# Performance work log

Hardware: AMD Instinct MI355X
Metric: run time of the kernel (lower is better)

Reference implementation:

```python
import jax, jax.numpy as jnp
import numpy as np

N, E, CIN, CHID, DIM, KS = 6000, 192000, 32, 64, 3, 5
K = KS ** DIM          # 125 total spline kernel weights
S = 2 ** DIM           # 8 nonzero linear B-spline basis products per edge


def spline_conv(x, edge_index, pseudo, W, root, bias):
    """SplineConv, degree-1 open B-spline, mean aggregation, root weight + bias.
    x: [N, Cin], edge_index: [2, E], pseudo: [E, DIM] in [0,1],
    W: [K, Cin, Cout], root: [Cin, Cout], bias: [Cout].
    """
    src, dst = edge_index[0], edge_index[1]
    cin = x.shape[1]
    # open spline: KS-1 intervals over [0,1]
    u = pseudo * (KS - 1)                               # [E, DIM]
    i0 = jnp.clip(jnp.floor(u), 0, KS - 2).astype(jnp.int32)
    frac = u - i0                                       # [E, DIM]
    bits = (jnp.arange(S)[:, None] >> jnp.arange(DIM)[None, :]) & 1   # [S, DIM]
    strides = KS ** jnp.arange(DIM - 1, -1, -1)         # row-major flattening
    idx = jnp.sum((i0[:, None, :] + bits[None, :, :]) * strides, axis=-1)  # [E, S]
    basis = jnp.prod(jnp.where(bits[None, :, :] == 1,
                               frac[:, None, :], 1.0 - frac[:, None, :]), axis=-1)  # [E, S]
    x_j = x[src]                                        # gather: [E, Cin]
    vals = (basis[..., None] * x_j[:, None, :]).reshape(E * S, cin)
    keys = (dst[:, None] * K + idx).reshape(E * S)
    # bucket basis-weighted source features per (dst node, kernel index)
    T = jax.ops.segment_sum(vals, keys, num_segments=N * K).reshape(N, K, cin)
    out = jnp.einsum('nki,kio->no', T, W)               # [N, Cout]
    deg = jax.ops.segment_sum(jnp.ones((E,), jnp.float32), dst, num_segments=N)
    out = out / jnp.maximum(deg, 1.0)[:, None]          # mean aggregation
    return out + x @ root + bias


def _conv_params(key, cin):
    k1, k2 = jax.random.split(key)
    w_scale = 1.0 / np.sqrt(cin * S)
    W = jax.random.normal(k1, (K, cin, CHID), jnp.float32) * w_scale
    root = jax.random.normal(k2, (cin, CHID), jnp.float32) * (1.0 / np.sqrt(cin))
    b = jnp.zeros((CHID,), jnp.float32)
    return W, root, b


def setup_inputs() -> dict:
    key = jax.random.key(0)
    ks = jax.random.split(key, 10)
    inp = {
        'x': jax.random.normal(ks[0], (N, CIN), jnp.float32),
        'hidden': jax.random.normal(ks[1], (N, CHID), jnp.float32),
        'edge_index': jax.random.randint(ks[2], (2, E), 0, N, dtype=jnp.int32),
        'edge_attr': jax.random.uniform(ks[3], (E, DIM), jnp.float32),
    }
    for i, (name, cin) in enumerate([('xr', CIN), ('hr', CHID), ('xz', CIN),
                                     ('hz', CHID), ('xn', CIN), ('hn', CHID)]):
        W, root, b = _conv_params(ks[4 + i], cin)
        inp[f'W_{name}'] = W
        inp[f'root_{name}'] = root
        inp[f'b_{name}'] = b
    return inp


def reference(x, hidden, edge_index, edge_attr,
              W_xr, root_xr, b_xr, W_hr, root_hr, b_hr,
              W_xz, root_xz, b_xz, W_hz, root_hz, b_hz,
              W_xn, root_xn, b_xn, W_hn, root_hn, b_hn):
    hr_out = spline_conv(hidden, edge_index, edge_attr, W_hr, root_hr, b_hr)
    r = jax.nn.sigmoid(spline_conv(x, edge_index, edge_attr, W_xr, root_xr, b_xr) + hr_out)
    z = jax.nn.sigmoid(spline_conv(x, edge_index, edge_attr, W_xz, root_xz, b_xz)
                       + spline_conv(hidden, edge_index, edge_attr, W_hz, root_hz, b_hz))
    # NOTE: the original torch forward reuses self.hr (not self.hn) here; replicated faithfully.
    n = jnp.tanh(spline_conv(x, edge_index, edge_attr, W_xn, root_xn, b_xn) + r * hr_out)
    h_new = (1.0 - z) * n + z * hidden
    return h_new
```

## Files before the change

### kernel.cpp

```cpp
#include <hip/hip_runtime.h>
#include <math.h>

#define NN_   6000
#define EE_   192000
#define CIN_  32
#define CHID_ 64
#define KK_   125
#define EB_   32
#define CH1_  4
#define CH2_  8
#define CPB_  16
#define MTILE_ 192

static __device__ __forceinline__ unsigned short f2bf(float f) {
    unsigned int u = __builtin_bit_cast(unsigned int, f);
    u += 0x7fff + ((u >> 16) & 1);
    return (unsigned short)(u >> 16);
}
static __device__ __forceinline__ float bf2f(unsigned short h) {
    unsigned int u = ((unsigned int)h) << 16;
    return __builtin_bit_cast(float, u);
}

#define PK1_ (192 * KK_ * CIN_)
#define PK2_ (128 * KK_ * CHID_)
#define CB_  ((EE_ + 255) / 256)
__global__ __launch_bounds__(256) void count_pack_kernel(
    const int* __restrict__ ei, int* __restrict__ deg,
    const float* __restrict__ W_xr, const float* __restrict__ W_xz,
    const float* __restrict__ W_xn, const float* __restrict__ W_hr,
    const float* __restrict__ W_hz,
    unsigned short* __restrict__ B1t, unsigned short* __restrict__ B2t)
{
    const int b = blockIdx.x;
    if (b < CB_) {
        int e = b * 256 + threadIdx.x;
        if (e < EE_) atomicAdd(&deg[ei[EE_ + e]], 1);
        return;
    }
    int gid = (b - CB_) * 256 + threadIdx.x;
    if (gid < PK1_) {
        int n  = gid / (KK_ * CIN_);
        int kk = gid % (KK_ * CIN_);
        int conv = n >> 6, o = n & 63;
        const float* W = (conv == 0) ? W_xr : ((conv == 1) ? W_xz : W_xn);
        B1t[gid] = f2bf(W[(size_t)kk * 64 + o]);
    } else if (gid < PK1_ + PK2_) {
        int g2 = gid - PK1_;
        int n  = g2 / (KK_ * CHID_);
        int kk = g2 % (KK_ * CHID_);
        int conv = n >> 6, o = n & 63;
        const float* W = (conv == 0) ? W_hr : W_hz;
        B2t[g2] = f2bf(W[(size_t)kk * 64 + o]);
    }
}

__global__ __launch_bounds__(1024) void scan_kernel(
    const int* __restrict__ deg, int* __restrict__ offs, int* __restrict__ cursor)
{
    __shared__ int part[1024];
    const int tid = threadIdx.x;
    const int CH = (NN_ + 1023) / 1024;
    const int base = tid * CH;
    int loc[CH];
    int s = 0;
#pragma unroll
    for (int i = 0; i < CH; ++i) {
        int v = (base + i < NN_) ? deg[base + i] : 0;
        loc[i] = s; s += v;
    }
    part[tid] = s;
    __syncthreads();
    for (int off = 1; off < 1024; off <<= 1) {
        int v = (tid >= off) ? part[tid - off] : 0;
        __syncthreads();
        part[tid] += v;
        __syncthreads();
    }
    const int pre = (tid > 0) ? part[tid - 1] : 0;
#pragma unroll
    for (int i = 0; i < CH; ++i) {
        if (base + i < NN_) {
            offs[base + i]   = pre + loc[i];
            cursor[base + i] = pre + loc[i];
        }
    }
    if (tid == 1023) offs[NN_] = part[1023];
}

__global__ __launch_bounds__(256) void prep_kernel(
    const int* __restrict__ ei, const float* __restrict__ attr,
    int* __restrict__ cursor, float4* __restrict__ meta_s, int* __restrict__ src_s)
{
    int e = blockIdx.x * 256 + threadIdx.x;
    if (e >= EE_) return;
    const int dst = ei[EE_ + e];
    const int p   = atomicAdd(&cursor[dst], 1);
    float f[3]; int i0[3];
#pragma unroll
    for (int d = 0; d < 3; ++d) {
        float u  = attr[e * 3 + d] * 4.0f;
        float fl = floorf(u);
        fl = fminf(fmaxf(fl, 0.0f), 3.0f);
        i0[d] = (int)fl;
        f[d]  = u - fl;
    }
    meta_s[p] = make_float4(f[0], f[1], f[2],
        __int_as_float(i0[0] * 25 + i0[1] * 5 + i0[2]));
    src_s[p] = ei[e];
}

template<int C>
__global__ __launch_bounds__(256) void build_T_kernel(
    const float4* __restrict__ meta_s, const int* __restrict__ src_s,
    const float* __restrict__ feat, const int* __restrict__ offs,
    unsigned short* __restrict__ Tb)
{
    constexpr int MP  = 40;
    constexpr int CT  = C / 16;
    constexpr int CPT = C / 8;
    using bf16x8 = __attribute__((ext_vector_type(8))) short;
    using f32x4  = __attribute__((ext_vector_type(4))) float;

    __shared__ __align__(16) unsigned short Mt [128 * MP];
    __shared__ __align__(16) unsigned short fbT[C   * MP];
    __shared__ int s_src[EB_];

    const int tid  = threadIdx.x;
    const int wave = tid >> 6;
    const int lane = tid & 63;
    const int quad = lane >> 4;
    const int l16  = lane & 15;
    const int node = blockIdx.x;

    for (int i = tid; i < C * MP / 8; i += 256)
        ((uint4*)fbT)[i] = make_uint4(0u, 0u, 0u, 0u);

    const int j0 = offs[node], j1 = offs[node + 1];

    f32x4 acc[2][CT];
#pragma unroll
    for (int t = 0; t < 2; ++t)
#pragma unroll
        for (int ct = 0; ct < CT; ++ct) acc[t][ct] = (f32x4){0.f, 0.f, 0.f, 0.f};

    for (int jb = j0; jb < j1; jb += EB_) {
        const int m = min(EB_, j1 - jb);

        __syncthreads();
        for (int i = tid; i < 128 * MP / 8; i += 256)
            ((uint4*)Mt)[i] = make_uint4(0u, 0u, 0u, 0u);
        if (tid < m) s_src[tid] = src_s[jb + tid];
        __syncthreads();

        if (tid < m) {
            const float4 mt = meta_s[jb + tid];
            const int base = __float_as_int(mt.w);
            const float f0 = mt.x, f1 = mt.y, f2 = mt.z;
            const float g0 = 1.f - f0, g1 = 1.f - f1, g2 = 1.f - f2;
            const float bb[8] = {g0*g1*g2, f0*g1*g2, g0*f1*g2, f0*f1*g2,
                                 g0*g1*f2, f0*g1*f2, g0*f1*f2, f0*f1*f2};
            const int oc[8] = {0, 25, 5, 30, 1, 26, 6, 31};
#pragma unroll
            for (int s = 0; s < 8; ++s)
                Mt[(base + oc[s]) * MP + tid] = f2bf(bb[s]);
        }
        {
            const int e = tid >> 3, cg = (tid & 7) * CPT;
            if (e < m) {
                const float* fr = &feat[(size_t)s_src[e] * C + cg];
#pragma unroll
                for (int c4 = 0; c4 < CPT; c4 += 4) {
                    float4 v = *(const float4*)(fr + c4);
                    fbT[(cg + c4 + 0) * MP + e] = f2bf(v.x);
                    fbT[(cg + c4 + 1) * MP + e] = f2bf(v.y);
                    fbT[(cg + c4 + 2) * MP + e] = f2bf(v.z);
                    fbT[(cg + c4 + 3) * MP + e] = f2bf(v.w);
                }
            }
        }
        __syncthreads();

        bf16x8 a0 = *(const bf16x8*)&Mt[((wave * 2 + 0) * 16 + l16) * MP + quad * 8];
        bf16x8 a1 = *(const bf16x8*)&Mt[((wave * 2 + 1) * 16 + l16) * MP + quad * 8];
#pragma unroll
        for (int ct = 0; ct < CT; ++ct) {
            bf16x8 b = *(const bf16x8*)&fbT[(ct * 16 + l16) * MP + quad * 8];
            acc[0][ct] = __builtin_amdgcn_mfma_f32_16x16x32_bf16(a0, b, acc[0][ct], 0, 0, 0);
            acc[1][ct] = __builtin_amdgcn_mfma_f32_16x16x32_bf16(a1, b, acc[1][ct], 0, 0, 0);
        }
    }

    unsigned short* To = Tb + (size_t)node * (KK_ * C);
#pragma unroll
    for (int t = 0; t < 2; ++t) {
        const int rbase = (wave * 2 + t) * 16 + quad * 4;
#pragma unroll
        for (int ct = 0; ct < CT; ++ct) {
#pragma unroll
            for (int r = 0; r < 4; ++r) {
                const int R = rbase + r;
                if (R < KK_) To[R * C + ct * 16 + l16] = f2bf(acc[t][ct][r]);
            }
        }
    }
}

template<int NT, int NTF, int CPB>
static __device__ __forceinline__ void gemm_body(
    unsigned char* arena,
    const unsigned short* __restrict__ A, const unsigned short* __restrict__ Bt,
    unsigned short* __restrict__ P, int M, int Kd, int chunk, int zhalf)
{
    constexpr int COLS   = 64;
    constexpr int RF     = 3;
    constexpr int NFRAG  = NT / 16;
    constexpr int CSP    = NT + 8;
    constexpr int ABYTES = MTILE_ * COLS * 2;
    constexpr int BBYTES = NT * COLS * 2;
    constexpr int AUNITS = MTILE_ * COLS / 8;
    constexpr int BUNITS = NT * COLS / 8;

    using bf16x8 = __attribute__((ext_vector_type(8))) short;
    using f32x4  = __attribute__((ext_vector_type(4))) float;

    unsigned short* As0 = (unsigned short*)(arena);
    unsigned short* As1 = (unsigned short*)(arena + ABYTES);
    unsigned short* Bs0 = (unsigned short*)(arena + 2 * ABYTES);
    unsigned short* Bs1 = (unsigned short*)(arena + 2 * ABYTES + BBYTES);

    const int tid  = threadIdx.x;
    const int wave = tid >> 6;
    const int lane = tid & 63;
    const int quad = lane >> 4;
    const int l16  = lane & 15;
    const int m0   = blockIdx.x * MTILE_;
    const unsigned short* Bp = Bt + (size_t)zhalf * NT * Kd;
    const int kbase = chunk * CPB * COLS;
    const int ccmax = min(CPB, (Kd - kbase + COLS - 1) / COLS);

    f32x4 acc[RF][NFRAG];
#pragma unroll
    for (int t = 0; t < RF; ++t)
#pragma unroll
        for (int f = 0; f < NFRAG; ++f) acc[t][f] = (f32x4){0.f, 0.f, 0.f, 0.f};

    auto STAGE = [&](int cc, unsigned short* Abuf, unsigned short* Bbuf) {
        const int k0 = kbase + cc * COLS;
#pragma unroll
        for (int i = 0; i < AUNITS / 256; ++i) {
            const int u    = tid + i * 256;
            const int row  = u >> 3;
            const int gblk = (u & 7) ^ (row & 7);
            const int k    = k0 + gblk * 8;
            if (k + 8 <= Kd) {
                const unsigned short* g = A + (size_t)(m0 + row) * Kd + k;
                __builtin_amdgcn_global_load_lds(
                    (const __attribute__((address_space(1))) void*)g,
                    (__attribute__((address_space(3))) void*)(Abuf + u * 8),
                    16, 0, 0);
            } else {
                *(uint4*)(Abuf + u * 8) = make_uint4(0u, 0u, 0u, 0u);
            }
        }
#pragma unroll
        for (int i = 0; i < BUNITS / 256; ++i) {
            const int u    = tid + i * 256;
            const int row  = u >> 3;
            const int gblk = (u & 7) ^ (row & 7);
            const unsigned short* g = Bp + (size_t)row * Kd + k0 + gblk * 8;
            __builtin_amdgcn_global_load_lds(
                (const __attribute__((address_space(1))) void*)g,
                (__attribute__((address_space(3))) void*)(Bbuf + u * 8),
                16, 0, 0);
        }
    };

    STAGE(0, As0, Bs0);
    __syncthreads();

    for (int cc = 0; cc < ccmax; ++cc) {
        unsigned short* Ac = (cc & 1) ? As1 : As0;
        unsigned short* Bc = (cc & 1) ? Bs1 : Bs0;
        if (cc + 1 < ccmax)
            STAGE(cc + 1, (cc & 1) ? As0 : As1, (cc & 1) ? Bs0 : Bs1);
#pragma unroll
        for (int s = 0; s < 2; ++s) {
            bf16x8 av[RF];
#pragma unroll
            for (int t = 0; t < RF; ++t) {
                const int row = (wave * RF + t) * 16 + l16;
                av[t] = *(const bf16x8*)
                    &Ac[row * COLS + (((s * 4 + quad) ^ (l16 & 7)) * 8)];
            }
#pragma unroll
            for (int f = 0; f < NFRAG; ++f) {
                bf16x8 bv = *(const bf16x8*)
                    &Bc[(f * 16 + l16) * COLS + (((s * 4 + quad) ^ (l16 & 7)) * 8)];
#pragma unroll
                for (int t = 0; t < RF; ++t)
                    acc[t][f] = __builtin_amdgcn_mfma_f32_16x16x32_bf16(
                        av[t], bv, acc[t][f], 0, 0, 0);
            }
        }
        __syncthreads();
    }

    unsigned short* Cs = (unsigned short*)arena;
    unsigned short* Pc = P + ((size_t)chunk * M + m0) * NTF + zhalf * NT;
#pragma unroll
    for (int p = 0; p < 3; ++p) {
        __syncthreads();
#pragma unroll
        for (int t = 0; t < RF; ++t) {
            const int fr = wave * RF + t;
            if ((fr >> 2) == p) {
                const int rb = (fr & 3) * 16 + quad * 4;
#pragma unroll
                for (int f = 0; f < NFRAG; ++f) {
                    const int col = f * 16 + l16;
#pragma unroll
                    for (int r = 0; r < 4; ++r)
                        Cs[(rb + r) * CSP + col] = f2bf(acc[t][f][r]);
                }
            }
        }
        __syncthreads();
        constexpr int UNITS = 64 * NT / 8;
        for (int u = tid; u < UNITS; u += 256) {
            const int row = (u * 8) / NT, col = (u * 8) % NT;
            if (m0 + p * 64 + row < M)
                *(uint4*)&Pc[(size_t)(p * 64 + row) * NTF + col] =
                    *(const uint4*)&Cs[row * CSP + col];
        }
    }
}

__global__ __launch_bounds__(256) void gemm_all_kernel(
    const unsigned short* __restrict__ Tx, const unsigned short* __restrict__ B1t,
    unsigned short* __restrict__ P1,
    const unsigned short* __restrict__ Th, const unsigned short* __restrict__ B2t,
    unsigned short* __restrict__ P2)
{
    __shared__ __align__(16) unsigned char arena[2 * 24576 + 2 * 16384];
    const int y = blockIdx.y;
    if (y < CH2_) {
        gemm_body<128, 128, CPB_>(arena, Th, B2t, P2, NN_, KK_ * CHID_, y, 0);
    } else {
        const int g = y - CH2_;
        gemm_body<96, 192, CPB_>(arena, Tx, B1t, P1, NN_, KK_ * CIN_, g >> 1, g & 1);
    }
}

__global__ __launch_bounds__(256) void epilogue_kernel(
    const unsigned short* __restrict__ P1, const unsigned short* __restrict__ P2,
    const int* __restrict__ offs,
    const float* __restrict__ x, const float* __restrict__ hidden,
    const float* __restrict__ root_xr, const float* __restrict__ root_hr,
    const float* __restrict__ root_xz, const float* __restrict__ root_hz,
    const float* __restrict__ root_xn,
    const float* __restrict__ b_xr, const float* __restrict__ b_hr,
    const float* __restrict__ b_xz, const float* __restrict__ b_hz,
    const float* __restrict__ b_xn,
    float* __restrict__ out)
{
    __shared__ float xsh[4][32];
    __shared__ float hsh[4][64];
    const int w = threadIdx.x >> 6;
    const int o = threadIdx.x & 63;
    const int m = blockIdx.x * 4 + w;
    if (m >= NN_) return;

    if (o < 32) xsh[w][o] = x[(size_t)m * 32 + o];
    const float hval = hidden[(size_t)m * 64 + o];
    hsh[w][o] = hval;

    float axr = 0.f, axz = 0.f, axn = 0.f;
#pragma unroll
    for (int c = 0; c < CH1_; ++c) {
        const unsigned short* p = P1 + ((size_t)c * NN_ + m) * 192;
        axr += bf2f(p[o]); axz += bf2f(p[64 + o]); axn += bf2f(p[128 + o]);
    }
    float ahr = 0.f, ahz = 0.f;
#pragma unroll
    for (int c = 0; c < CH2_; ++c) {
        const unsigned short* p = P2 + ((size_t)c * NN_ + m) * 128;
        ahr += bf2f(p[o]); ahz += bf2f(p[64 + o]);
    }

    const int   dg   = offs[m + 1] - offs[m];
    const float dinv = 1.0f / fmaxf((float)dg, 1.0f);
    axr *= dinv; axz *= dinv; axn *= dinv; ahr *= dinv; ahz *= dinv;

    float sxr = 0.f, sxz = 0.f, sxn = 0.f;
#pragma unroll
    for (int c = 0; c < CIN_; ++c) {
        float xv = xsh[w][c];
        sxr += xv * root_xr[c * 64 + o];
        sxz += xv * root_xz[c * 64 + o];
        sxn += xv * root_xn[c * 64 + o];
    }
    float shr = 0.f, shz = 0.f;
#pragma unroll
    for (int c = 0; c < CHID_; ++c) {
        float hv = hsh[w][c];
        shr += hv * root_hr[c * 64 + o];
        shz += hv * root_hz[c * 64 + o];
    }

    const float conv_xr = axr + sxr + b_xr[o];
    const float conv_xz = axz + sxz + b_xz[o];
    const float conv_xn = axn + sxn + b_xn[o];
    const float hr_out  = ahr + shr + b_hr[o];
    const float conv_hz = ahz + shz + b_hz[o];

    const float rg = 1.0f / (1.0f + expf(-(conv_xr + hr_out)));
    const float zg = 1.0f / (1.0f + expf(-(conv_xz + conv_hz)));
    const float ng = tanhf(conv_xn + rg * hr_out);
    out[(size_t)m * 64 + o] = (1.0f - zg) * ng + zg * hval;
}

extern "C" void kernel_launch(void* const* d_in, const int* in_sizes, int n_in,
                              void* d_out, int out_size, void* d_ws, size_t ws_size,
                              hipStream_t stream)
{
    const float* x       = (const float*)d_in[0];
    const float* hidden  = (const float*)d_in[1];
    const int*   ei      = (const int*)  d_in[2];
    const float* attr    = (const float*)d_in[3];
    const float* W_xr    = (const float*)d_in[4];
    const float* root_xr = (const float*)d_in[5];
    const float* b_xr    = (const float*)d_in[6];
    const float* W_hr    = (const float*)d_in[7];
    const float* root_hr = (const float*)d_in[8];
    const float* b_hr    = (const float*)d_in[9];
    const float* W_xz    = (const float*)d_in[10];
    const float* root_xz = (const float*)d_in[11];
    const float* b_xz    = (const float*)d_in[12];
    const float* W_hz    = (const float*)d_in[13];
    const float* root_hz = (const float*)d_in[14];
    const float* b_hz    = (const float*)d_in[15];
    const float* W_xn    = (const float*)d_in[16];
    const float* root_xn = (const float*)d_in[17];
    const float* b_xn    = (const float*)d_in[18];
    float* out = (float*)d_out;

    char* w = (char*)d_ws;
    unsigned short* Tx  = (unsigned short*)w; w += (size_t)NN_ * KK_ * CIN_  * 2;
    unsigned short* Th  = (unsigned short*)w; w += (size_t)NN_ * KK_ * CHID_ * 2;
    unsigned short* B1t = (unsigned short*)w; w += (size_t)192 * KK_ * CIN_  * 2;
    unsigned short* B2t = (unsigned short*)w; w += (size_t)128 * KK_ * CHID_ * 2;
    unsigned short* P1  = (unsigned short*)w; w += (size_t)CH1_ * NN_ * 192 * 2;
    unsigned short* P2  = (unsigned short*)w; w += (size_t)CH2_ * NN_ * 128 * 2;
    float4* meta_s = (float4*)w; w += (size_t)EE_ * 16;
    int* src_s  = (int*)w;   w += (size_t)EE_ * 4;
    int* deg    = (int*)w;   w += (size_t)NN_ * 4;
    int* offs   = (int*)w;   w += (size_t)(NN_ + 4) * 4;
    int* cursor = (int*)w;   w += (size_t)NN_ * 4;

    const int MT = (NN_ + MTILE_ - 1) / MTILE_;

    hipMemsetAsync(deg, 0, (size_t)NN_ * 4, stream);

    const int PACKB = (PK1_ + PK2_ + 255) / 256;
    count_pack_kernel<<<CB_ + PACKB, 256, 0, stream>>>(
        ei, deg, W_xr, W_xz, W_xn, W_hr, W_hz, B1t, B2t);

    scan_kernel<<<1, 1024, 0, stream>>>(deg, offs, cursor);
    prep_kernel<<<(EE_ + 255) / 256, 256, 0, stream>>>(ei, attr, cursor, meta_s, src_s);

    build_T_kernel<CHID_><<<NN_, 256, 0, stream>>>(meta_s, src_s, hidden, offs, Th);
    build_T_kernel<CIN_><<<NN_, 256, 0, stream>>>(meta_s, src_s, x, offs, Tx);

    gemm_all_kernel<<<dim3(MT, CH2_ + 2 * CH1_), 256, 0, stream>>>(
        Tx, B1t, P1, Th, B2t, P2);

    epilogue_kernel<<<(NN_ + 3) / 4, 256, 0, stream>>>(
        P1, P2, offs, x, hidden,
        root_xr, root_hr, root_xz, root_hz, root_xn,
        b_xr, b_hr, b_xz, b_hz, b_xn, out);
}
```

Before: 249.9 us.

## Triple-buffer GEMM LDS staging with explicit vmcnt waits and zero-pad loads

The GEMM main loop moves from double buffering to a three-slot LDS ring with two stages in flight. It uses explicit s_waitcnt vmcnt counts plus raw barriers in place of __syncthreads. Out-of-range A tiles now load from a zeroed global pad through global_load_lds instead of writing zeros to LDS directly, which keeps the per-stage load count uniform for the vmcnt arithmetic. This is meant to hide global-to-LDS latency better, at the cost of more LDS per block (about 120KB), which may lower occupancy, and the fragility of hand-counted wait values.

```diff
diff --git a/kernel.cpp b/kernel.cpp
--- a/kernel.cpp
+++ b/kernel.cpp
@@ -20,6 +20,11 @@
 static __device__ __forceinline__ float bf2f(unsigned short h) {
     unsigned int u = ((unsigned int)h) << 16;
     return __builtin_bit_cast(float, u);
+}
+
+template<int N> static __device__ __forceinline__ void vwait() {
+    asm volatile("s_waitcnt vmcnt(%0)" :: "n"(N) : "memory");
+    __builtin_amdgcn_sched_barrier(0);
 }
 
 #define PK1_ (192 * KK_ * CIN_)
@@ -206,28 +211,24 @@
     }
 }
 
-template<int NT, int NTF, int CPB>
+template<int NT, int NTF, int CPB, int LW>
 static __device__ __forceinline__ void gemm_body(
-    unsigned char* arena,
+    unsigned short* arena,
     const unsigned short* __restrict__ A, const unsigned short* __restrict__ Bt,
+    const unsigned short* __restrict__ zp,
     unsigned short* __restrict__ P, int M, int Kd, int chunk, int zhalf)
 {
     constexpr int COLS   = 64;
     constexpr int RF     = 3;
     constexpr int NFRAG  = NT / 16;
     constexpr int CSP    = NT + 8;
-    constexpr int ABYTES = MTILE_ * COLS * 2;
-    constexpr int BBYTES = NT * COLS * 2;
+    constexpr int ASH    = MTILE_ * COLS;
+    constexpr int SLOT   = ASH + 128 * COLS;
     constexpr int AUNITS = MTILE_ * COLS / 8;
     constexpr int BUNITS = NT * COLS / 8;
 
     using bf16x8 = __attribute__((ext_vector_type(8))) short;
     using f32x4  = __attribute__((ext_vector_type(4))) float;
-
-    unsigned short* As0 = (unsigned short*)(arena);
-    unsigned short* As1 = (unsigned short*)(arena + ABYTES);
-    unsigned short* Bs0 = (unsigned short*)(arena + 2 * ABYTES);
-    unsigned short* Bs1 = (unsigned short*)(arena + 2 * ABYTES + BBYTES);
 
     const int tid  = threadIdx.x;
     const int wave = tid >> 6;
@@ -245,7 +246,9 @@
 #pragma unroll
         for (int f = 0; f < NFRAG; ++f) acc[t][f] = (f32x4){0.f, 0.f, 0.f, 0.f};
 
-    auto STAGE = [&](int cc, unsigned short* Abuf, unsigned short* Bbuf) {
+    auto STAGE = [&](int cc, int slot) {
+        unsigned short* Abuf = arena + slot * SLOT;
+        unsigned short* Bbuf = Abuf + ASH;
         const int k0 = kbase + cc * COLS;
 #pragma unroll
         for (int i = 0; i < AUNITS / 256; ++i) {
@@ -253,15 +256,13 @@
             const int row  = u >> 3;
             const int gblk = (u & 7) ^ (row & 7);
             const int k    = k0 + gblk * 8;
-            if (k + 8 <= Kd) {
-                const unsigned short* g = A + (size_t)(m0 + row) * Kd + k;
-                __builtin_amdgcn_global_load_lds(
-                    (const __attribute__((address_space(1))) void*)g,
-                    (__attribute__((address_space(3))) void*)(Abuf + u * 8),
-                    16, 0, 0);
-            } else {
-                *(uint4*)(Abuf + u * 8) = make_uint4(0u, 0u, 0u, 0u);
-            }
+            const unsigned short* g = (k + 8 <= Kd)
+                ? A + (size_t)(m0 + row) * Kd + k
+                : zp + (u & 3) * 8;
+            __builtin_amdgcn_global_load_lds(
+                (const __attribute__((address_space(1))) void*)g,
+                (__attribute__((address_space(3))) void*)(Abuf + u * 8),
+                16, 0, 0);
         }
 #pragma unroll
         for (int i = 0; i < BUNITS / 256; ++i) {
@@ -276,14 +277,22 @@
         }
     };
 
-    STAGE(0, As0, Bs0);
-    __syncthreads();
+    STAGE(0, 0);
+    STAGE(1, 1);
 
     for (int cc = 0; cc < ccmax; ++cc) {
-        unsigned short* Ac = (cc & 1) ? As1 : As0;
-        unsigned short* Bc = (cc & 1) ? Bs1 : Bs0;
-        if (cc + 1 < ccmax)
-            STAGE(cc + 1, (cc & 1) ? As0 : As1, (cc & 1) ? Bs0 : Bs1);
+        asm volatile("" ::: "memory");
+        __builtin_amdgcn_s_barrier();
+        if (cc + 2 < ccmax) STAGE(cc + 2, (cc + 2) % 3);
+        const int ahead = min(2, ccmax - 1 - cc);
+        if      (ahead == 2) vwait<2 * LW>();
+        else if (ahead == 1) vwait<LW>();
+        else                 vwait<0>();
+        __builtin_amdgcn_s_barrier();
+        asm volatile("" ::: "memory");
+
+        const unsigned short* Ac = arena + (cc % 3) * SLOT;
+        const unsigned short* Bc = Ac + ASH;
 #pragma unroll
         for (int s = 0; s < 2; ++s) {
             bf16x8 av[RF];
@@ -303,10 +312,9 @@
                         av[t], bv, acc[t][f], 0, 0, 0);
             }
         }
-        __syncthreads();
-    }
-
-    unsigned short* Cs = (unsigned short*)arena;
+    }
+
+    unsigned short* Cs = arena;
     unsigned short* Pc = P + ((size_t)chunk * M + m0) * NTF + zhalf * NT;
 #pragma unroll
     for (int p = 0; p < 3; ++p) {
@@ -340,15 +348,15 @@
     const unsigned short* __restrict__ Tx, const unsigned short* __restrict__ B1t,
     unsigned short* __restrict__ P1,
     const unsigned short* __restrict__ Th, const unsigned short* __restrict__ B2t,
-    unsigned short* __restrict__ P2)
-{
-    __shared__ __align__(16) unsigned char arena[2 * 24576 + 2 * 16384];
+    unsigned short* __restrict__ P2, const unsigned short* __restrict__ zp)
+{
+    __shared__ __align__(16) unsigned short arena[3 * 20480];
     const int y = blockIdx.y;
     if (y < CH2_) {
-        gemm_body<128, 128, CPB_>(arena, Th, B2t, P2, NN_, KK_ * CHID_, y, 0);
+        gemm_body<128, 128, CPB_, 10>(arena, Th, B2t, zp, P2, NN_, KK_ * CHID_, y, 0);
     } else {
         const int g = y - CH2_;
-        gemm_body<96, 192, CPB_>(arena, Tx, B1t, P1, NN_, KK_ * CIN_, g >> 1, g & 1);
+        gemm_body<96, 192, CPB_, 9>(arena, Tx, B1t, zp, P1, NN_, KK_ * CIN_, g >> 1, g & 1);
     }
 }
 
@@ -457,10 +465,12 @@
     int* deg    = (int*)w;   w += (size_t)NN_ * 4;
     int* offs   = (int*)w;   w += (size_t)(NN_ + 4) * 4;
     int* cursor = (int*)w;   w += (size_t)NN_ * 4;
+    unsigned short* zpad = (unsigned short*)w; w += 256;
 
     const int MT = (NN_ + MTILE_ - 1) / MTILE_;
 
     hipMemsetAsync(deg, 0, (size_t)NN_ * 4, stream);
+    hipMemsetAsync(zpad, 0, 256, stream);
 
     const int PACKB = (PK1_ + PK2_ + 255) / 256;
     count_pack_kernel<<<CB_ + PACKB, 256, 0, stream>>>(
@@ -473,7 +483,7 @@
     build_T_kernel<CIN_><<<NN_, 256, 0, stream>>>(meta_s, src_s, x, offs, Tx);
 
     gemm_all_kernel<<<dim3(MT, CH2_ + 2 * CH1_), 256, 0, stream>>>(
-        Tx, B1t, P1, Th, B2t, P2);
+        Tx, B1t, P1, Th, B2t, P2, zpad);
 
     epilogue_kernel<<<(NN_ + 3) / 4, 256, 0, stream>>>(
         P1, P2, offs, x, hidden,
```

Result: no change. 245.2 us (-1.9%).
